# Kernel optimization log

Measured on AMD Instinct MI355X. Metric: run time of the kernel, lower is better.

## Reference

```python
import jax, jax.numpy as jnp
import numpy as np

N = 50000      # nodes
E = 800000     # edges (before self-loops)
IN_DIM = 128
OUT_DIM = 64   # per-head channels C (concat=False)
HEADS = 4
NEG_SLOPE = 0.2


def setup_inputs() -> dict:
    key = jax.random.key(0)
    ks = jax.random.split(key, 10)
    x = jax.random.normal(ks[0], (N, IN_DIM), dtype=jnp.float32)
    edge_index = jax.random.randint(ks[1], (2, E), 0, N, dtype=jnp.int32)
    # GAT parameters
    W = jax.random.normal(ks[2], (IN_DIM, HEADS * OUT_DIM), dtype=jnp.float32) * 0.05
    att_src = jax.random.normal(ks[3], (HEADS, OUT_DIM), dtype=jnp.float32) * 0.05
    att_dst = jax.random.normal(ks[4], (HEADS, OUT_DIM), dtype=jnp.float32) * 0.05
    bias = jnp.zeros((OUT_DIM,), dtype=jnp.float32)
    # LayerNorm + PReLU parameters
    gamma = jnp.ones((OUT_DIM,), dtype=jnp.float32)
    beta = jnp.zeros((OUT_DIM,), dtype=jnp.float32)
    prelu_w = jnp.full((1,), 0.25, dtype=jnp.float32)
    return {"x": x, "edge_index": edge_index, "W": W, "att_src": att_src,
            "att_dst": att_dst, "bias": bias, "gamma": gamma, "beta": beta,
            "prelu_w": prelu_w}


def reference(x, edge_index, W, att_src, att_dst, bias, gamma, beta, prelu_w):
    n = x.shape[0]
    # PyG GATConv default add_self_loops=True
    loops = jnp.arange(n, dtype=edge_index.dtype)
    src = jnp.concatenate([edge_index[0], loops])  # message sources j
    dst = jnp.concatenate([edge_index[1], loops])  # message targets i

    # linear projection into heads: [N, H, C]
    h = (x @ W).reshape(n, HEADS, OUT_DIM)
    a_src = jnp.einsum('nhc,hc->nh', h, att_src)  # [N, H]
    a_dst = jnp.einsum('nhc,hc->nh', h, att_dst)  # [N, H]

    # per-edge attention logits, leaky relu
    alpha = a_src[src] + a_dst[dst]                       # [E', H]
    alpha = jnp.where(alpha >= 0, alpha, NEG_SLOPE * alpha)

    # segment softmax over incoming edges of each destination node
    amax = jax.ops.segment_max(alpha, dst, num_segments=n)   # [N, H]
    e = jnp.exp(alpha - amax[dst])
    denom = jax.ops.segment_sum(e, dst, num_segments=n)      # [N, H]
    w = e / denom[dst]                                       # [E', H]

    # weighted scatter-aggregate of messages
    msg = h[src] * w[:, :, None]                             # [E', H, C]
    out = jax.ops.segment_sum(msg, dst, num_segments=n)      # [N, H, C]

    # concat=False -> mean over heads, then bias
    out = out.mean(axis=1) + bias                            # [N, C]

    # LayerNorm
    mu = out.mean(axis=-1, keepdims=True)
    var = out.var(axis=-1, keepdims=True)
    out = (out - mu) * jax.lax.rsqrt(var + 1e-5) * gamma + beta

    # PReLU (single shared weight)
    return jnp.where(out >= 0, out, prelu_w[0] * out)
```

## Files before the change

kernel.cpp:

```cpp
#include <hip/hip_runtime.h>

#define HEADS 4
#define CDIM  64
#define INDIM 128
#define NEG   0.2f
#define CAP     256
#define FASTCAP 252
#define NPB     256

typedef __attribute__((ext_vector_type(8))) short short8;
typedef __attribute__((ext_vector_type(4))) float f32x4;
typedef _Float16 half2_t __attribute__((ext_vector_type(2)));

__device__ __forceinline__ float wave_sum(float v) {
#pragma unroll
    for (int o = 32; o > 0; o >>= 1) v += __shfl_xor(v, o, 64);
    return v;
}
__device__ __forceinline__ int wave_sum_i(int v) {
#pragma unroll
    for (int o = 32; o > 0; o >>= 1) v += __shfl_xor(v, o, 64);
    return v;
}

__device__ __forceinline__ unsigned short f2bf(float f) {
    unsigned u = __float_as_uint(f);
    u = (u + 0x7FFFu + ((u >> 16) & 1u)) >> 16;
    return (unsigned short)u;
}

__device__ __forceinline__ unsigned pk_f16(float a, float b) {
    auto h = __builtin_amdgcn_cvt_pkrtz(a, b);
    return __builtin_bit_cast(unsigned, h);
}
__device__ __forceinline__ half2_t as_h2(unsigned u) {
    return __builtin_bit_cast(half2_t, u);
}

#if __has_builtin(__builtin_amdgcn_fdot2)
__device__ __forceinline__ float fdot2(unsigned a, unsigned b, float c) {
    return __builtin_amdgcn_fdot2(as_h2(a), as_h2(b), c, false);
}
#else
__device__ __forceinline__ float fdot2(unsigned a, unsigned b, float c) {
    half2_t ha = as_h2(a), hb = as_h2(b);
    return c + (float)ha.x * (float)hb.x + (float)ha.y * (float)hb.y;
}
#endif

__device__ __forceinline__ float lrelu(float a) { return a >= 0.f ? a : NEG * a; }

__global__ __launch_bounds__(256) void k_prep(const float* __restrict__ W,
    const float* __restrict__ att_src, const float* __restrict__ att_dst,
    unsigned short* __restrict__ Waug)
{
    const int wv = threadIdx.x >> 6, lane = threadIdx.x & 63;
    const int c = blockIdx.x * 4 + wv;
    if (c >= 272) return;
#pragma unroll
    for (int kk = 0; kk < 2; ++kk) {
        int k = lane + kk * 64;
        float val;
        if (c < 256) {
            val = W[k * 256 + c];
        } else if (c < 260) {
            int q = c - 256; float s = 0.f;
            for (int j = 0; j < 64; ++j) s += W[k * 256 + q * 64 + j] * att_src[q * 64 + j];
            val = s;
        } else if (c < 264) {
            int q = c - 260; float s = 0.f;
            for (int j = 0; j < 64; ++j) s += W[k * 256 + q * 64 + j] * att_dst[q * 64 + j];
            val = s;
        } else {
            val = 0.f;
        }
        Waug[c * 128 + k] = f2bf(val);
    }
}

__global__ __launch_bounds__(512) void gemm_mfma(
    const float* __restrict__ x, const unsigned short* __restrict__ Waug,
    uint2* __restrict__ hp, float* __restrict__ a_src, float* __restrict__ a_dst,
    int N)
{
    extern __shared__ char smem[];
    const int t = threadIdx.x;

    const uint4* srcw = (const uint4*)Waug;
    for (int i = t; i < 272 * 16; i += 512) {
        int col = i >> 4, kc = i & 15;
        int off = col * 256 + ((kc * 16) ^ ((col & 7) << 4));
        *(uint4*)(smem + off) = srcw[i];
    }
    __syncthreads();

    const int lane = t & 63, wv = t >> 6;
    const int l = lane & 15, g = lane >> 4;
    const int rowbase = blockIdx.x * 128 + wv * 16;

    int anode = rowbase + l; if (anode >= N) anode = N - 1;
    const float4* xrow = (const float4*)(x + (size_t)anode * INDIM);

    short8 af[4];
#pragma unroll
    for (int ks = 0; ks < 4; ++ks) {
        float4 x0 = xrow[ks * 8 + g * 2];
        float4 x1 = xrow[ks * 8 + g * 2 + 1];
        short8 a;
        a[0] = (short)f2bf(x0.x); a[1] = (short)f2bf(x0.y);
        a[2] = (short)f2bf(x0.z); a[3] = (short)f2bf(x0.w);
        a[4] = (short)f2bf(x1.x); a[5] = (short)f2bf(x1.y);
        a[6] = (short)f2bf(x1.z); a[7] = (short)f2bf(x1.w);
        af[ks] = a;
    }

    f32x4 acc[17];
    const f32x4 zero = {0.f, 0.f, 0.f, 0.f};
#pragma unroll
    for (int tt = 0; tt < 17; ++tt) acc[tt] = zero;

    const int base_b = l * 256;
#pragma unroll
    for (int ks = 0; ks < 4; ++ks) {
        const int koff = (ks * 64 + g * 16) ^ ((l & 7) << 4);
#pragma unroll
        for (int tt = 0; tt < 17; ++tt) {
            short8 bf = *(const short8*)(smem + tt * 4096 + base_b + koff);
            acc[tt] = __builtin_amdgcn_mfma_f32_16x16x32_bf16(af[ks], bf, acc[tt], 0, 0, 0);
        }
    }

#pragma unroll
    for (int j = 0; j < 4; ++j) {
        int node = rowbase + g * 4 + j;
        if (node < N) {
#pragma unroll
            for (int u = 0; u < 4; ++u) {
                int ch = l + 16 * u;
                hp[(size_t)node * CDIM + ch] = make_uint2(
                    pk_f16(acc[u][j],     acc[4 + u][j]),
                    pk_f16(acc[8 + u][j], acc[12 + u][j]));
            }
            if (l < 4)      a_src[node * 4 + l]       = acc[16][j];
            else if (l < 8) a_dst[node * 4 + (l - 4)] = acc[16][j];
        }
    }
}


__global__ __launch_bounds__(256) void k_count(const int* __restrict__ ei,
    int E, int EPB, int NBUK, int* __restrict__ counts)
{
    __shared__ int hist[256];
    const int t = threadIdx.x, blk = blockIdx.x;
    if (t < NBUK) hist[t] = 0;
    __syncthreads();
    const int e0 = blk * EPB;
    for (int j = t; j < EPB; j += 256) {
        int e = e0 + j;
        if (e < E) atomicAdd(&hist[ei[E + e] >> 8], 1);
    }
    __syncthreads();
    if (t < NBUK) counts[t * NPB + blk] = hist[t];
}

__global__ __launch_bounds__(256) void k_scan1(const int* __restrict__ arr,
    int* __restrict__ bsum, int n)
{
    const int t = threadIdx.x, lane = t & 63, wv = t >> 6;
    int gid = blockIdx.x * 256 + t;
    int v = (gid < n) ? arr[gid] : 0;
    v = wave_sum_i(v);
    __shared__ int ws[4];
    if (lane == 0) ws[wv] = v;
    __syncthreads();
    if (t == 0) bsum[blockIdx.x] = ws[0] + ws[1] + ws[2] + ws[3];
}

__global__ __launch_bounds__(1024) void k_scan2(int* __restrict__ bsum, int NB)
{
    __shared__ int lds[1024];
    const int t = threadIdx.x;
    int v = (t < NB) ? bsum[t] : 0;
    lds[t] = v;
    __syncthreads();
    for (int o = 1; o < 1024; o <<= 1) {
        int u = (t >= o) ? lds[t - o] : 0;
        __syncthreads();
        lds[t] += u;
        __syncthreads();
    }
    if (t < NB) bsum[t] = lds[t] - v;
}

__global__ __launch_bounds__(256) void k_scanip(int* __restrict__ arr,
    const int* __restrict__ bsum, int n)
{
    const int t = threadIdx.x, lane = t & 63, wv = t >> 6;
    int gid = blockIdx.x * 256 + t;
    int v = (gid < n) ? arr[gid] : 0;
    int inc = v;
#pragma unroll
    for (int o = 1; o < 64; o <<= 1) {
        int u = __shfl_up(inc, o, 64);
        if (lane >= o) inc += u;
    }
    __shared__ int wtot[4];
    if (lane == 63) wtot[wv] = inc;
    __syncthreads();
    int wpre = 0;
    for (int w = 0; w < wv; ++w) wpre += wtot[w];
    int ex = inc - v + wpre + bsum[blockIdx.x];
    if (gid < n) arr[gid] = ex;
}

__global__ __launch_bounds__(256) void k_part(const int* __restrict__ ei,
    int E, int EPB, int NBUK, const int* __restrict__ counts,
    uint2* __restrict__ srt)
{
    __shared__ int cb[256];
    const int t = threadIdx.x, blk = blockIdx.x;
    if (t < NBUK) cb[t] = counts[t * NPB + blk];
    __syncthreads();
    const int e0 = blk * EPB;
    for (int j = t; j < EPB; j += 256) {
        int e = e0 + j;
        if (e < E) {
            int s = ei[e], d = ei[E + e];
            int pos = atomicAdd(&cb[d >> 8], 1);
            srt[pos] = make_uint2((unsigned)s, (unsigned)d);
        }
    }
}

__global__ __launch_bounds__(256) void k_bcsr(const uint2* __restrict__ srt,
    const int* __restrict__ counts, int E, int N, int NBUK,
    int* __restrict__ deg, int* __restrict__ off, int* __restrict__ csr)
{
    __shared__ int h[256];
    __shared__ int cur[256];
    __shared__ int wt[4];
    const int t = threadIdx.x, b = blockIdx.x;
    const int bb0 = counts[b * NPB];
    const int bb1 = (b + 1 < NBUK) ? counts[(b + 1) * NPB] : E;
    const int ne = bb1 - bb0;

    h[t] = 0;
    __syncthreads();
    for (int j = t; j < ne; j += 256) atomicAdd(&h[srt[bb0 + j].y & 255], 1);
    __syncthreads();

    int v = h[t];
    const int lane = t & 63, wv = t >> 6;
    int inc = v;
#pragma unroll
    for (int o = 1; o < 64; o <<= 1) {
        int u = __shfl_up(inc, o, 64);
        if (lane >= o) inc += u;
    }
    if (lane == 63) wt[wv] = inc;
    __syncthreads();
    int wpre = 0;
    for (int w = 0; w < wv; ++w) wpre += wt[w];
    int ex = inc - v + wpre;

    int node = (b << 8) + t;
    if (node < N) { deg[node] = v; off[node] = bb0 + ex; }
    cur[t] = bb0 + ex;
    __syncthreads();

    for (int j = t; j < ne; j += 256) {
        uint2 u = srt[bb0 + j];
        int pos = atomicAdd(&cur[u.y & 255], 1);
        csr[pos] = (int)u.x;
    }
}

__global__ __launch_bounds__(256) void aggr_fused(
    const int* __restrict__ off, const int* __restrict__ deg,
    const int* __restrict__ csr_src,
    const float4* __restrict__ a_src4, const float4* __restrict__ a_dst4,
    const uint2* __restrict__ hp,
    const float* __restrict__ bias, const float* __restrict__ gamma,
    const float* __restrict__ beta, const float* __restrict__ prelu,
    float* __restrict__ out, int N)
{
    __shared__ uint4 slot[4][CAP];
    const int wv   = threadIdx.x >> 6;
    const int lane = threadIdx.x & 63;
    const int wid  = (int)(blockIdx.x * 4u + wv);
    if (wid >= N) return;
    const int d = wid;
    uint4* sl = slot[wv];

    const float4 ad = a_dst4[d];
    const int deg_d = deg[d];
    const int beg   = off[d];
    const int nv    = deg_d < FASTCAP ? deg_d : FASTCAP;
    const int nv4   = (nv + 3) & ~3;

    float dl0 = 0.f, dl1 = 0.f, dl2 = 0.f, dl3 = 0.f;
    for (int base = 0; base < deg_d; base += 64) {
        int j = base + lane;
        bool valid = j < deg_d;
        int sv = valid ? csr_src[beg + j] : 0;
        float4 as = a_src4[sv];
        float e0 = valid ? __expf(lrelu(as.x + ad.x)) : 0.f;
        float e1 = valid ? __expf(lrelu(as.y + ad.y)) : 0.f;
        float e2 = valid ? __expf(lrelu(as.z + ad.z)) : 0.f;
        float e3 = valid ? __expf(lrelu(as.w + ad.w)) : 0.f;
        dl0 += e0; dl1 += e1; dl2 += e2; dl3 += e3;
        if (j < CAP) sl[j] = make_uint4(pk_f16(e0, e1), pk_f16(e2, e3), (unsigned)sv, 0u);
    }

    float4 asd = a_src4[d];
    float es0 = __expf(lrelu(asd.x + ad.x));
    float es1 = __expf(lrelu(asd.y + ad.y));
    float es2 = __expf(lrelu(asd.z + ad.z));
    float es3 = __expf(lrelu(asd.w + ad.w));

    float r0 = __builtin_amdgcn_rcpf(wave_sum(dl0) + es0);
    float r1 = __builtin_amdgcn_rcpf(wave_sum(dl1) + es1);
    float r2 = __builtin_amdgcn_rcpf(wave_sum(dl2) + es2);
    float r3 = __builtin_amdgcn_rcpf(wave_sum(dl3) + es3);

    for (int base = 0; base < nv4; base += 64) {
        int j = base + lane;
        if (j < nv) {
            uint2 ev = *(const uint2*)&sl[j];
            half2_t e01 = as_h2(ev.x), e23 = as_h2(ev.y);
            *(uint2*)&sl[j] = make_uint2(
                pk_f16((float)e01.x * r0, (float)e01.y * r1),
                pk_f16((float)e23.x * r2, (float)e23.y * r3));
        } else if (j < nv4) {
            sl[j] = make_uint4(0u, 0u, 0u, 0u);
        }
    }
    __builtin_amdgcn_wave_barrier();

    uint2 hd = hp[(size_t)d * CDIM + lane];
    unsigned pw01 = pk_f16(es0 * r0, es1 * r1);
    unsigned pw23 = pk_f16(es2 * r2, es3 * r3);
    float acc01 = fdot2(pw01, hd.x, 0.f);
    float acc23 = fdot2(pw23, hd.y, 0.f);

    if (nv4 >= 8) {
        uint4 c0 = sl[0], c1 = sl[1], c2 = sl[2], c3 = sl[3];
        uint2 h0 = hp[(size_t)c0.z * CDIM + lane];
        uint2 h1 = hp[(size_t)c1.z * CDIM + lane];
        uint2 h2 = hp[(size_t)c2.z * CDIM + lane];
        uint2 h3 = hp[(size_t)c3.z * CDIM + lane];
        int j = 0;
        for (; j + 7 < nv4; j += 4) {
            uint4 n0 = sl[j + 4], n1 = sl[j + 5], n2 = sl[j + 6], n3 = sl[j + 7];
            uint2 g0 = hp[(size_t)n0.z * CDIM + lane];
            uint2 g1 = hp[(size_t)n1.z * CDIM + lane];
            uint2 g2 = hp[(size_t)n2.z * CDIM + lane];
            uint2 g3 = hp[(size_t)n3.z * CDIM + lane];
            acc01 = fdot2(c0.x, h0.x, acc01); acc23 = fdot2(c0.y, h0.y, acc23);
            acc01 = fdot2(c1.x, h1.x, acc01); acc23 = fdot2(c1.y, h1.y, acc23);
            acc01 = fdot2(c2.x, h2.x, acc01); acc23 = fdot2(c2.y, h2.y, acc23);
            acc01 = fdot2(c3.x, h3.x, acc01); acc23 = fdot2(c3.y, h3.y, acc23);
            c0 = n0; c1 = n1; c2 = n2; c3 = n3;
            h0 = g0; h1 = g1; h2 = g2; h3 = g3;
        }
        acc01 = fdot2(c0.x, h0.x, acc01); acc23 = fdot2(c0.y, h0.y, acc23);
        acc01 = fdot2(c1.x, h1.x, acc01); acc23 = fdot2(c1.y, h1.y, acc23);
        acc01 = fdot2(c2.x, h2.x, acc01); acc23 = fdot2(c2.y, h2.y, acc23);
        acc01 = fdot2(c3.x, h3.x, acc01); acc23 = fdot2(c3.y, h3.y, acc23);
    } else if (nv4 == 4) {
        uint4 c0 = sl[0], c1 = sl[1], c2 = sl[2], c3 = sl[3];
        uint2 h0 = hp[(size_t)c0.z * CDIM + lane];
        uint2 h1 = hp[(size_t)c1.z * CDIM + lane];
        uint2 h2 = hp[(size_t)c2.z * CDIM + lane];
        uint2 h3 = hp[(size_t)c3.z * CDIM + lane];
        acc01 = fdot2(c0.x, h0.x, acc01); acc23 = fdot2(c0.y, h0.y, acc23);
        acc01 = fdot2(c1.x, h1.x, acc01); acc23 = fdot2(c1.y, h1.y, acc23);
        acc01 = fdot2(c2.x, h2.x, acc01); acc23 = fdot2(c2.y, h2.y, acc23);
        acc01 = fdot2(c3.x, h3.x, acc01); acc23 = fdot2(c3.y, h3.y, acc23);
    }

    for (int base = FASTCAP; base < deg_d; base += 64) {
        int jj = base + lane;
        bool valid = jj < deg_d;
        int sv = valid ? csr_src[beg + jj] : 0;
        float4 as = a_src4[sv];
        float e0 = valid ? __expf(lrelu(as.x + ad.x)) : 0.f;
        float e1 = valid ? __expf(lrelu(as.y + ad.y)) : 0.f;
        float e2 = valid ? __expf(lrelu(as.z + ad.z)) : 0.f;
        float e3 = valid ? __expf(lrelu(as.w + ad.w)) : 0.f;
        sl[lane] = make_uint4(pk_f16(e0 * r0, e1 * r1), pk_f16(e2 * r2, e3 * r3),
                              (unsigned)sv, 0u);
        __builtin_amdgcn_wave_barrier();
        int nav = deg_d - base; if (nav > 64) nav = 64;
        for (int q = 0; q < nav; ++q) {
            uint4 t0 = sl[q];
            uint2 h0 = hp[(size_t)t0.z * CDIM + lane];
            acc01 = fdot2(t0.x, h0.x, acc01);
            acc23 = fdot2(t0.y, h0.y, acc23);
        }
        __builtin_amdgcn_wave_barrier();
    }

    float v = 0.25f * (acc01 + acc23) + bias[lane];
    float mu  = wave_sum(v) * (1.f / 64.f);
    float df  = v - mu;
    float var = wave_sum(df * df) * (1.f / 64.f);
    float rs  = rsqrtf(var + 1e-5f);
    float o   = df * rs * gamma[lane] + beta[lane];
    float pw  = prelu[0];
    o = o >= 0.f ? o : pw * o;
    out[(size_t)d * CDIM + lane] = o;
}

extern "C" void kernel_launch(void* const* d_in, const int* in_sizes, int n_in,
                              void* d_out, int out_size, void* d_ws, size_t ws_size,
                              hipStream_t stream)
{
    const float* x       = (const float*)d_in[0];
    const int*   ei      = (const int*)  d_in[1];
    const float* W       = (const float*)d_in[2];
    const float* att_src = (const float*)d_in[3];
    const float* att_dst = (const float*)d_in[4];
    const float* bias    = (const float*)d_in[5];
    const float* gamma   = (const float*)d_in[6];
    const float* beta    = (const float*)d_in[7];
    const float* prelu   = (const float*)d_in[8];

    const int N = in_sizes[0] / INDIM;
    const int E = in_sizes[1] / 2;
    float* out = (float*)d_out;

    const int NBUK = (N + 255) >> 8;
    const int EPB  = (E + NPB - 1) / NPB;
    const int NCNT = NBUK * NPB;

    uint2* hp     = (uint2*)d_ws;
    float* a_src  = (float*)(hp + (size_t)N * CDIM);
    float* a_dst  = a_src + (size_t)N * HEADS;
    int*   deg    = (int*)(a_dst + (size_t)N * HEADS);
    int*   off    = deg + N;
    int*   counts = off + N;
    int*   bsum   = counts + NCNT;
    uint2* srt    = (uint2*)(bsum + 1024);
    int*   csr    = (int*)(srt + E);
    unsigned short* Waug = (unsigned short*)(csr + E);

    k_prep<<<68, 256, 0, stream>>>(W, att_src, att_dst, Waug);

    k_count<<<NPB, 256, 0, stream>>>(ei, E, EPB, NBUK, counts);
    k_scan1<<<NBUK, 256, 0, stream>>>(counts, bsum, NCNT);
    k_scan2<<<1, 1024, 0, stream>>>(bsum, NBUK);
    k_scanip<<<NBUK, 256, 0, stream>>>(counts, bsum, NCNT);
    k_part<<<NPB, 256, 0, stream>>>(ei, E, EPB, NBUK, counts, srt);
    k_bcsr<<<NBUK, 256, 0, stream>>>(srt, counts, E, N, NBUK, deg, off, csr);

    gemm_mfma<<<(N + 127) / 128, 512, 69632, stream>>>(
        x, Waug, hp, a_src, a_dst, N);

    aggr_fused<<<(N + 3) / 4, 256, 0, stream>>>(
        off, deg, csr, (const float4*)a_src, (const float4*)a_dst, hp,
        bias, gamma, beta, prelu, out, N);
}
```

Measured before the change: 119.6 us.

## Fuse prep with count, merge scan passes, pack sort keys, defer softmax normalization

```diff
diff --git a/kernel.cpp b/kernel.cpp
--- a/kernel.cpp
+++ b/kernel.cpp
@@ -37,29 +37,39 @@
     return __builtin_bit_cast(half2_t, u);
 }
 
-#if __has_builtin(__builtin_amdgcn_fdot2)
-__device__ __forceinline__ float fdot2(unsigned a, unsigned b, float c) {
-    return __builtin_amdgcn_fdot2(as_h2(a), as_h2(b), c, false);
-}
-#else
-__device__ __forceinline__ float fdot2(unsigned a, unsigned b, float c) {
-    half2_t ha = as_h2(a), hb = as_h2(b);
-    return c + (float)ha.x * (float)hb.x + (float)ha.y * (float)hb.y;
-}
-#endif
-
 __device__ __forceinline__ float lrelu(float a) { return a >= 0.f ? a : NEG * a; }
 
-__global__ __launch_bounds__(256) void k_prep(const float* __restrict__ W,
-    const float* __restrict__ att_src, const float* __restrict__ att_dst,
-    unsigned short* __restrict__ Waug)
-{
-    const int wv = threadIdx.x >> 6, lane = threadIdx.x & 63;
-    const int c = blockIdx.x * 4 + wv;
-    if (c >= 272) return;
-#pragma unroll
-    for (int kk = 0; kk < 2; ++kk) {
-        int k = lane + kk * 64;
+__device__ __forceinline__ void acc_edge(uint4 c, uint2 h,
+    float& a0, float& a1, float& a2, float& a3)
+{
+    half2_t e01 = as_h2(c.x), e23 = as_h2(c.y);
+    half2_t h01 = as_h2(h.x), h23 = as_h2(h.y);
+    a0 = fmaf((float)e01.x, (float)h01.x, a0);
+    a1 = fmaf((float)e01.y, (float)h01.y, a1);
+    a2 = fmaf((float)e23.x, (float)h23.x, a2);
+    a3 = fmaf((float)e23.y, (float)h23.y, a3);
+}
+
+__global__ __launch_bounds__(256) void k_count_prep(const int* __restrict__ ei,
+    int E, int EPB, int NBUK, int* __restrict__ counts,
+    const float* __restrict__ W, const float* __restrict__ att_src,
+    const float* __restrict__ att_dst, unsigned short* __restrict__ Waug)
+{
+    __shared__ int hist[256];
+    const int t = threadIdx.x, blk = blockIdx.x;
+    hist[t] = 0;
+    __syncthreads();
+    const int e0 = blk * EPB;
+    for (int j = t; j < EPB; j += 256) {
+        int e = e0 + j;
+        if (e < E) atomicAdd(&hist[ei[E + e] >> 8], 1);
+    }
+    __syncthreads();
+    if (t < NBUK) counts[t * NPB + blk] = hist[t];
+
+    int idx = blk * 256 + t;
+    if (idx < 272 * 128) {
+        int c = idx >> 7, k = idx & 127;
         float val;
         if (c < 256) {
             val = W[k * 256 + c];
@@ -78,6 +88,112 @@
     }
 }
 
+__global__ __launch_bounds__(256) void k_scan1(const int* __restrict__ arr,
+    int* __restrict__ bsum, int n)
+{
+    const int t = threadIdx.x, lane = t & 63, wv = t >> 6;
+    int gid = blockIdx.x * 256 + t;
+    int v = (gid < n) ? arr[gid] : 0;
+    v = wave_sum_i(v);
+    __shared__ int ws[4];
+    if (lane == 0) ws[wv] = v;
+    __syncthreads();
+    if (t == 0) bsum[blockIdx.x] = ws[0] + ws[1] + ws[2] + ws[3];
+}
+
+__global__ __launch_bounds__(256) void k_scanip2(int* __restrict__ arr,
+    const int* __restrict__ bsum, int NB, int n)
+{
+    __shared__ int wred[4];
+    __shared__ int wtot[4];
+    __shared__ int spre;
+    const int t = threadIdx.x, lane = t & 63, wv = t >> 6, b = blockIdx.x;
+
+    int u0 = (t < NB && t < b) ? bsum[t] : 0;
+    u0 = wave_sum_i(u0);
+    if (lane == 0) wred[wv] = u0;
+    __syncthreads();
+    if (t == 0) spre = wred[0] + wred[1] + wred[2] + wred[3];
+    __syncthreads();
+
+    int gid = b * 256 + t;
+    int v = (gid < n) ? arr[gid] : 0;
+    int inc = v;
+#pragma unroll
+    for (int o = 1; o < 64; o <<= 1) {
+        int u = __shfl_up(inc, o, 64);
+        if (lane >= o) inc += u;
+    }
+    if (lane == 63) wtot[wv] = inc;
+    __syncthreads();
+    int wpre = 0;
+    for (int w = 0; w < wv; ++w) wpre += wtot[w];
+    int ex = inc - v + wpre + spre;
+    if (gid < n) arr[gid] = ex;
+}
+
+__global__ __launch_bounds__(256) void k_part(const int* __restrict__ ei,
+    int E, int EPB, int NBUK, const int* __restrict__ counts,
+    unsigned* __restrict__ srt)
+{
+    __shared__ int cb[256];
+    const int t = threadIdx.x, blk = blockIdx.x;
+    if (t < NBUK) cb[t] = counts[t * NPB + blk];
+    __syncthreads();
+    const int e0 = blk * EPB;
+    for (int j = t; j < EPB; j += 256) {
+        int e = e0 + j;
+        if (e < E) {
+            int s = ei[e], d = ei[E + e];
+            int pos = atomicAdd(&cb[d >> 8], 1);
+            srt[pos] = ((unsigned)s << 8) | ((unsigned)d & 255u);
+        }
+    }
+}
+
+__global__ __launch_bounds__(256) void k_bcsr(const unsigned* __restrict__ srt,
+    const int* __restrict__ counts, int E, int N, int NBUK,
+    int* __restrict__ deg, int* __restrict__ off, int* __restrict__ csr)
+{
+    __shared__ int h[256];
+    __shared__ int cur[256];
+    __shared__ int wt[4];
+    const int t = threadIdx.x, b = blockIdx.x;
+    const int bb0 = counts[b * NPB];
+    const int bb1 = (b + 1 < NBUK) ? counts[(b + 1) * NPB] : E;
+    const int ne = bb1 - bb0;
+
+    h[t] = 0;
+    __syncthreads();
+    for (int j = t; j < ne; j += 256) atomicAdd(&h[srt[bb0 + j] & 255u], 1);
+    __syncthreads();
+
+    int v = h[t];
+    const int lane = t & 63, wv = t >> 6;
+    int inc = v;
+#pragma unroll
+    for (int o = 1; o < 64; o <<= 1) {
+        int u = __shfl_up(inc, o, 64);
+        if (lane >= o) inc += u;
+    }
+    if (lane == 63) wt[wv] = inc;
+    __syncthreads();
+    int wpre = 0;
+    for (int w = 0; w < wv; ++w) wpre += wt[w];
+    int ex = inc - v + wpre;
+
+    int node = (b << 8) + t;
+    if (node < N) { deg[node] = v; off[node] = bb0 + ex; }
+    cur[t] = bb0 + ex;
+    __syncthreads();
+
+    for (int j = t; j < ne; j += 256) {
+        unsigned u = srt[bb0 + j];
+        int pos = atomicAdd(&cur[u & 255u], 1);
+        csr[pos] = (int)(u >> 8);
+    }
+}
+
 __global__ __launch_bounds__(512) void gemm_mfma(
     const float* __restrict__ x, const unsigned short* __restrict__ Waug,
     uint2* __restrict__ hp, float* __restrict__ a_src, float* __restrict__ a_dst,
@@ -147,135 +263,6 @@
     }
 }
 
-
-__global__ __launch_bounds__(256) void k_count(const int* __restrict__ ei,
-    int E, int EPB, int NBUK, int* __restrict__ counts)
-{
-    __shared__ int hist[256];
-    const int t = threadIdx.x, blk = blockIdx.x;
-    if (t < NBUK) hist[t] = 0;
-    __syncthreads();
-    const int e0 = blk * EPB;
-    for (int j = t; j < EPB; j += 256) {
-        int e = e0 + j;
-        if (e < E) atomicAdd(&hist[ei[E + e] >> 8], 1);
-    }
-    __syncthreads();
-    if (t < NBUK) counts[t * NPB + blk] = hist[t];
-}
-
-__global__ __launch_bounds__(256) void k_scan1(const int* __restrict__ arr,
-    int* __restrict__ bsum, int n)
-{
-    const int t = threadIdx.x, lane = t & 63, wv = t >> 6;
-    int gid = blockIdx.x * 256 + t;
-    int v = (gid < n) ? arr[gid] : 0;
-    v = wave_sum_i(v);
-    __shared__ int ws[4];
-    if (lane == 0) ws[wv] = v;
-    __syncthreads();
-    if (t == 0) bsum[blockIdx.x] = ws[0] + ws[1] + ws[2] + ws[3];
-}
-
-__global__ __launch_bounds__(1024) void k_scan2(int* __restrict__ bsum, int NB)
-{
-    __shared__ int lds[1024];
-    const int t = threadIdx.x;
-    int v = (t < NB) ? bsum[t] : 0;
-    lds[t] = v;
-    __syncthreads();
-    for (int o = 1; o < 1024; o <<= 1) {
-        int u = (t >= o) ? lds[t - o] : 0;
-        __syncthreads();
-        lds[t] += u;
-        __syncthreads();
-    }
-    if (t < NB) bsum[t] = lds[t] - v;
-}
-
-__global__ __launch_bounds__(256) void k_scanip(int* __restrict__ arr,
-    const int* __restrict__ bsum, int n)
-{
-    const int t = threadIdx.x, lane = t & 63, wv = t >> 6;
-    int gid = blockIdx.x * 256 + t;
-    int v = (gid < n) ? arr[gid] : 0;
-    int inc = v;
-#pragma unroll
-    for (int o = 1; o < 64; o <<= 1) {
-        int u = __shfl_up(inc, o, 64);
-        if (lane >= o) inc += u;
-    }
-    __shared__ int wtot[4];
-    if (lane == 63) wtot[wv] = inc;
-    __syncthreads();
-    int wpre = 0;
-    for (int w = 0; w < wv; ++w) wpre += wtot[w];
-    int ex = inc - v + wpre + bsum[blockIdx.x];
-    if (gid < n) arr[gid] = ex;
-}
-
-__global__ __launch_bounds__(256) void k_part(const int* __restrict__ ei,
-    int E, int EPB, int NBUK, const int* __restrict__ counts,
-    uint2* __restrict__ srt)
-{
-    __shared__ int cb[256];
-    const int t = threadIdx.x, blk = blockIdx.x;
-    if (t < NBUK) cb[t] = counts[t * NPB + blk];
-    __syncthreads();
-    const int e0 = blk * EPB;
-    for (int j = t; j < EPB; j += 256) {
-        int e = e0 + j;
-        if (e < E) {
-            int s = ei[e], d = ei[E + e];
-            int pos = atomicAdd(&cb[d >> 8], 1);
-            srt[pos] = make_uint2((unsigned)s, (unsigned)d);
-        }
-    }
-}
-
-__global__ __launch_bounds__(256) void k_bcsr(const uint2* __restrict__ srt,
-    const int* __restrict__ counts, int E, int N, int NBUK,
-    int* __restrict__ deg, int* __restrict__ off, int* __restrict__ csr)
-{
-    __shared__ int h[256];
-    __shared__ int cur[256];
-    __shared__ int wt[4];
-    const int t = threadIdx.x, b = blockIdx.x;
-    const int bb0 = counts[b * NPB];
-    const int bb1 = (b + 1 < NBUK) ? counts[(b + 1) * NPB] : E;
-    const int ne = bb1 - bb0;
-
-    h[t] = 0;
-    __syncthreads();
-    for (int j = t; j < ne; j += 256) atomicAdd(&h[srt[bb0 + j].y & 255], 1);
-    __syncthreads();
-
-    int v = h[t];
-    const int lane = t & 63, wv = t >> 6;
-    int inc = v;
-#pragma unroll
-    for (int o = 1; o < 64; o <<= 1) {
-        int u = __shfl_up(inc, o, 64);
-        if (lane >= o) inc += u;
-    }
-    if (lane == 63) wt[wv] = inc;
-    __syncthreads();
-    int wpre = 0;
-    for (int w = 0; w < wv; ++w) wpre += wt[w];
-    int ex = inc - v + wpre;
-
-    int node = (b << 8) + t;
-    if (node < N) { deg[node] = v; off[node] = bb0 + ex; }
-    cur[t] = bb0 + ex;
-    __syncthreads();
-
-    for (int j = t; j < ne; j += 256) {
-        uint2 u = srt[bb0 + j];
-        int pos = atomicAdd(&cur[u.y & 255], 1);
-        csr[pos] = (int)u.x;
-    }
-}
-
 __global__ __launch_bounds__(256) void aggr_fused(
     const int* __restrict__ off, const int* __restrict__ deg,
     const int* __restrict__ csr_src,
@@ -293,7 +280,11 @@
     const int d = wid;
     uint4* sl = slot[wv];
 
-    const float4 ad = a_dst4[d];
+    const float bl = bias[lane], gl = gamma[lane], bt = beta[lane], pw = prelu[0];
+    const float4 ad  = a_dst4[d];
+    const float4 asd = a_src4[d];
+    const uint2  hd  = hp[(size_t)d * CDIM + lane];
+
     const int deg_d = deg[d];
     const int beg   = off[d];
     const int nv    = deg_d < FASTCAP ? deg_d : FASTCAP;
@@ -310,46 +301,37 @@
         float e2 = valid ? __expf(lrelu(as.z + ad.z)) : 0.f;
         float e3 = valid ? __expf(lrelu(as.w + ad.w)) : 0.f;
         dl0 += e0; dl1 += e1; dl2 += e2; dl3 += e3;
-        if (j < CAP) sl[j] = make_uint4(pk_f16(e0, e1), pk_f16(e2, e3), (unsigned)sv, 0u);
-    }
-
-    float4 asd = a_src4[d];
+        if (j < nv4) sl[j] = make_uint4(pk_f16(e0, e1), pk_f16(e2, e3),
+                                        valid ? (unsigned)sv : 0u, 0u);
+    }
+    __builtin_amdgcn_wave_barrier();
+
     float es0 = __expf(lrelu(asd.x + ad.x));
     float es1 = __expf(lrelu(asd.y + ad.y));
     float es2 = __expf(lrelu(asd.z + ad.z));
     float es3 = __expf(lrelu(asd.w + ad.w));
 
-    float r0 = __builtin_amdgcn_rcpf(wave_sum(dl0) + es0);
-    float r1 = __builtin_amdgcn_rcpf(wave_sum(dl1) + es1);
-    float r2 = __builtin_amdgcn_rcpf(wave_sum(dl2) + es2);
-    float r3 = __builtin_amdgcn_rcpf(wave_sum(dl3) + es3);
-
-    for (int base = 0; base < nv4; base += 64) {
-        int j = base + lane;
-        if (j < nv) {
-            uint2 ev = *(const uint2*)&sl[j];
-            half2_t e01 = as_h2(ev.x), e23 = as_h2(ev.y);
-            *(uint2*)&sl[j] = make_uint2(
-                pk_f16((float)e01.x * r0, (float)e01.y * r1),
-                pk_f16((float)e23.x * r2, (float)e23.y * r3));
-        } else if (j < nv4) {
-            sl[j] = make_uint4(0u, 0u, 0u, 0u);
-        }
-    }
-    __builtin_amdgcn_wave_barrier();
-
-    uint2 hd = hp[(size_t)d * CDIM + lane];
-    unsigned pw01 = pk_f16(es0 * r0, es1 * r1);
-    unsigned pw23 = pk_f16(es2 * r2, es3 * r3);
-    float acc01 = fdot2(pw01, hd.x, 0.f);
-    float acc23 = fdot2(pw23, hd.y, 0.f);
-
-    if (nv4 >= 8) {
-        uint4 c0 = sl[0], c1 = sl[1], c2 = sl[2], c3 = sl[3];
-        uint2 h0 = hp[(size_t)c0.z * CDIM + lane];
-        uint2 h1 = hp[(size_t)c1.z * CDIM + lane];
-        uint2 h2 = hp[(size_t)c2.z * CDIM + lane];
-        uint2 h3 = hp[(size_t)c3.z * CDIM + lane];
+    float a0 = 0.f, a1 = 0.f, a2 = 0.f, a3 = 0.f;
+    uint4 c0, c1, c2, c3;
+    uint2 h0, h1, h2, h3;
+    if (nv4 >= 4) {
+        c0 = sl[0]; c1 = sl[1]; c2 = sl[2]; c3 = sl[3];
+        h0 = hp[(size_t)c0.z * CDIM + lane];
+        h1 = hp[(size_t)c1.z * CDIM + lane];
+        h2 = hp[(size_t)c2.z * CDIM + lane];
+        h3 = hp[(size_t)c3.z * CDIM + lane];
+    }
+
+    float den0 = wave_sum(dl0) + es0;
+    float den1 = wave_sum(dl1) + es1;
+    float den2 = wave_sum(dl2) + es2;
+    float den3 = wave_sum(dl3) + es3;
+    float r0 = __builtin_amdgcn_rcpf(den0);
+    float r1 = __builtin_amdgcn_rcpf(den1);
+    float r2 = __builtin_amdgcn_rcpf(den2);
+    float r3 = __builtin_amdgcn_rcpf(den3);
+
+    if (nv4 >= 4) {
         int j = 0;
         for (; j + 7 < nv4; j += 4) {
             uint4 n0 = sl[j + 4], n1 = sl[j + 5], n2 = sl[j + 6], n3 = sl[j + 7];
@@ -357,27 +339,17 @@
             uint2 g1 = hp[(size_t)n1.z * CDIM + lane];
             uint2 g2 = hp[(size_t)n2.z * CDIM + lane];
             uint2 g3 = hp[(size_t)n3.z * CDIM + lane];
-            acc01 = fdot2(c0.x, h0.x, acc01); acc23 = fdot2(c0.y, h0.y, acc23);
-            acc01 = fdot2(c1.x, h1.x, acc01); acc23 = fdot2(c1.y, h1.y, acc23);
-            acc01 = fdot2(c2.x, h2.x, acc01); acc23 = fdot2(c2.y, h2.y, acc23);
-            acc01 = fdot2(c3.x, h3.x, acc01); acc23 = fdot2(c3.y, h3.y, acc23);
+            acc_edge(c0, h0, a0, a1, a2, a3);
+            acc_edge(c1, h1, a0, a1, a2, a3);
+            acc_edge(c2, h2, a0, a1, a2, a3);
+            acc_edge(c3, h3, a0, a1, a2, a3);
             c0 = n0; c1 = n1; c2 = n2; c3 = n3;
             h0 = g0; h1 = g1; h2 = g2; h3 = g3;
         }
-        acc01 = fdot2(c0.x, h0.x, acc01); acc23 = fdot2(c0.y, h0.y, acc23);
-        acc01 = fdot2(c1.x, h1.x, acc01); acc23 = fdot2(c1.y, h1.y, acc23);
-        acc01 = fdot2(c2.x, h2.x, acc01); acc23 = fdot2(c2.y, h2.y, acc23);
-        acc01 = fdot2(c3.x, h3.x, acc01); acc23 = fdot2(c3.y, h3.y, acc23);
-    } else if (nv4 == 4) {
-        uint4 c0 = sl[0], c1 = sl[1], c2 = sl[2], c3 = sl[3];
-        uint2 h0 = hp[(size_t)c0.z * CDIM + lane];
-        uint2 h1 = hp[(size_t)c1.z * CDIM + lane];
-        uint2 h2 = hp[(size_t)c2.z * CDIM + lane];
-        uint2 h3 = hp[(size_t)c3.z * CDIM + lane];
-        acc01 = fdot2(c0.x, h0.x, acc01); acc23 = fdot2(c0.y, h0.y, acc23);
-        acc01 = fdot2(c1.x, h1.x, acc01); acc23 = fdot2(c1.y, h1.y, acc23);
-        acc01 = fdot2(c2.x, h2.x, acc01); acc23 = fdot2(c2.y, h2.y, acc23);
-        acc01 = fdot2(c3.x, h3.x, acc01); acc23 = fdot2(c3.y, h3.y, acc23);
+        acc_edge(c0, h0, a0, a1, a2, a3);
+        acc_edge(c1, h1, a0, a1, a2, a3);
+        acc_edge(c2, h2, a0, a1, a2, a3);
+        acc_edge(c3, h3, a0, a1, a2, a3);
     }
 
     for (int base = FASTCAP; base < deg_d; base += 64) {
@@ -389,26 +361,30 @@
         float e1 = valid ? __expf(lrelu(as.y + ad.y)) : 0.f;
         float e2 = valid ? __expf(lrelu(as.z + ad.z)) : 0.f;
         float e3 = valid ? __expf(lrelu(as.w + ad.w)) : 0.f;
-        sl[lane] = make_uint4(pk_f16(e0 * r0, e1 * r1), pk_f16(e2 * r2, e3 * r3),
-                              (unsigned)sv, 0u);
+        sl[lane] = make_uint4(pk_f16(e0, e1), pk_f16(e2, e3),
+                              valid ? (unsigned)sv : 0u, 0u);
         __builtin_amdgcn_wave_barrier();
         int nav = deg_d - base; if (nav > 64) nav = 64;
         for (int q = 0; q < nav; ++q) {
             uint4 t0 = sl[q];
-            uint2 h0 = hp[(size_t)t0.z * CDIM + lane];
-            acc01 = fdot2(t0.x, h0.x, acc01);
-            acc23 = fdot2(t0.y, h0.y, acc23);
+            uint2 hq = hp[(size_t)t0.z * CDIM + lane];
+            acc_edge(t0, hq, a0, a1, a2, a3);
         }
         __builtin_amdgcn_wave_barrier();
     }
 
-    float v = 0.25f * (acc01 + acc23) + bias[lane];
+    half2_t hd01 = as_h2(hd.x), hd23 = as_h2(hd.y);
+    a0 = fmaf(es0, (float)hd01.x, a0);
+    a1 = fmaf(es1, (float)hd01.y, a1);
+    a2 = fmaf(es2, (float)hd23.x, a2);
+    a3 = fmaf(es3, (float)hd23.y, a3);
+
+    float v = 0.25f * (a0 * r0 + a1 * r1 + a2 * r2 + a3 * r3) + bl;
     float mu  = wave_sum(v) * (1.f / 64.f);
     float df  = v - mu;
     float var = wave_sum(df * df) * (1.f / 64.f);
     float rs  = rsqrtf(var + 1e-5f);
-    float o   = df * rs * gamma[lane] + beta[lane];
-    float pw  = prelu[0];
+    float o   = df * rs * gl + bt;
     o = o >= 0.f ? o : pw * o;
     out[(size_t)d * CDIM + lane] = o;
 }
@@ -435,23 +411,21 @@
     const int EPB  = (E + NPB - 1) / NPB;
     const int NCNT = NBUK * NPB;
 
-    uint2* hp     = (uint2*)d_ws;
-    float* a_src  = (float*)(hp + (size_t)N * CDIM);
-    float* a_dst  = a_src + (size_t)N * HEADS;
-    int*   deg    = (int*)(a_dst + (size_t)N * HEADS);
-    int*   off    = deg + N;
-    int*   counts = off + N;
-    int*   bsum   = counts + NCNT;
-    uint2* srt    = (uint2*)(bsum + 1024);
-    int*   csr    = (int*)(srt + E);
+    uint2*    hp     = (uint2*)d_ws;
+    float*    a_src  = (float*)(hp + (size_t)N * CDIM);
+    float*    a_dst  = a_src + (size_t)N * HEADS;
+    int*      deg    = (int*)(a_dst + (size_t)N * HEADS);
+    int*      off    = deg + N;
+    int*      counts = off + N;
+    int*      bsum   = counts + NCNT;
+    unsigned* srt    = (unsigned*)(bsum + 1024);
+    int*      csr    = (int*)(srt + E);
     unsigned short* Waug = (unsigned short*)(csr + E);
 
-    k_prep<<<68, 256, 0, stream>>>(W, att_src, att_dst, Waug);
-
-    k_count<<<NPB, 256, 0, stream>>>(ei, E, EPB, NBUK, counts);
+    k_count_prep<<<NPB, 256, 0, stream>>>(ei, E, EPB, NBUK, counts,
+                                          W, att_src, att_dst, Waug);
     k_scan1<<<NBUK, 256, 0, stream>>>(counts, bsum, NCNT);
-    k_scan2<<<1, 1024, 0, stream>>>(bsum, NBUK);
-    k_scanip<<<NBUK, 256, 0, stream>>>(counts, bsum, NCNT);
+    k_scanip2<<<NBUK, 256, 0, stream>>>(counts, bsum, NBUK, NCNT);
     k_part<<<NPB, 256, 0, stream>>>(ei, E, EPB, NBUK, counts, srt);
     k_bcsr<<<NBUK, 256, 0, stream>>>(srt, counts, E, N, NBUK, deg, off, csr);
 
```

New measurement: 114.6 us. 4.2% less time.
